# Optimization experiments

Measured on AMD Instinct MI355X. Metric: run time of the kernel, lower is better.

The kernel has to match this reference:

```python
import jax, jax.numpy as jnp
import numpy as np

B, L, H, DK, DV = 4, 2048, 8, 64, 64


def setup_inputs() -> dict:
    key = jax.random.key(0)
    ks = jax.random.split(key, 5)
    s = 0.05
    return {
        "x": jax.random.normal(ks[0], (B, L, DV), dtype=jnp.float32),
        "wq": jax.random.normal(ks[1], (DV, H * DK), dtype=jnp.float32) * s,
        "bq": jnp.zeros((H * DK,), dtype=jnp.float32),
        "wk": jax.random.normal(ks[2], (DV, H * DK), dtype=jnp.float32) * s,
        "bk": jnp.zeros((H * DK,), dtype=jnp.float32),
        "wv": jax.random.normal(ks[3], (DV, H * DV), dtype=jnp.float32) * s,
        "bv": jnp.zeros((H * DV,), dtype=jnp.float32),
        "wo": jax.random.normal(ks[4], (H * DV, DV), dtype=jnp.float32) * s,
        "bo": jnp.zeros((DV,), dtype=jnp.float32),
    }


def reference(x, wq, bq, wk, bk, wv, bv, wo, bo):
    b, l, _ = x.shape
    # QKV projections -> [B, H, L, d]
    q = (x @ wq + bq).reshape(b, l, H, DK).transpose(0, 2, 1, 3)
    k = (x @ wk + bk).reshape(b, l, H, DK).transpose(0, 2, 1, 3)
    v = (x @ wv + bv).reshape(b, l, H, DV).transpose(0, 2, 1, 3)
    # NOTE: original MULTIPLIES by sqrt(dk) (a quirk), not divides.
    align = jnp.einsum('bhqd,bhkd->bhqk', q, k) * jnp.sqrt(jnp.float32(DK))
    align = jax.nn.softmax(align, axis=-1)
    # Equivalent to the tile/multiply/reduce_sum: sum_k align[...,k] * v[...,k,:]
    ctx = jnp.einsum('bhqk,bhkv->bhqv', align, v)  # [B, H, L, DV]
    # NOTE: original transposes to [B, L, DV, H] before flattening (dv-major).
    ctx = ctx.transpose(0, 2, 3, 1).reshape(b, l, DV * H)
    return ctx @ wo + bo
```

## Files before the change

kernel.cpp:

```cpp
#include <hip/hip_runtime.h>


typedef _Float16 half4v __attribute__((ext_vector_type(4)));
typedef _Float16 half8v __attribute__((ext_vector_type(8)));
typedef float    float4v __attribute__((ext_vector_type(4)));

#define BB   4
#define LL   2048
#define HH   8
#define DKV  64
#define NROW (BB * LL)
#define QSCALE 11.541560327111707f

#define KVBLK 64
#define NKB   (LL / KVBLK)

#define GLOAD_LDS(gp, sp) \
    __builtin_amdgcn_global_load_lds((const __attribute__((address_space(1))) void*)(gp), \
                                     (__attribute__((address_space(3))) void*)(sp), 16, 0, 0)

__global__ __launch_bounds__(256) void k_prep_x(const float* __restrict__ x,
                                                _Float16* __restrict__ xh) {
    int i = blockIdx.x * 256 + threadIdx.x;
    float4v v = ((const float4v*)x)[i];
    half4v h;
    h[0] = (_Float16)v[0]; h[1] = (_Float16)v[1];
    h[2] = (_Float16)v[2]; h[3] = (_Float16)v[3];
    ((half4v*)xh)[i] = h;
}

__global__ __launch_bounds__(256) void k_prep_w(const float* __restrict__ wq, const float* __restrict__ bq,
                                                const float* __restrict__ wk, const float* __restrict__ bk,
                                                const float* __restrict__ wv, const float* __restrict__ bv,
                                                _Float16* __restrict__ wt, float* __restrict__ biasc) {
    int idx = blockIdx.x * 256 + threadIdx.x;
    int j = idx >> 6, i = idx & 63;
    const float* w; const float* bsrc; int jj; float sc = 1.0f;
    if (j < 512)       { w = wq; bsrc = bq; jj = j;        sc = QSCALE; }
    else if (j < 1024) { w = wk; bsrc = bk; jj = j - 512;  }
    else               { w = wv; bsrc = bv; jj = j - 1024; }
    wt[idx] = (_Float16)(w[i * 512 + jj] * sc);
    if (i == 0) biasc[j] = bsrc[jj] * sc;
}

__global__ __launch_bounds__(256) void k_prep_wo(const float* __restrict__ wo,
                                                 _Float16* __restrict__ wo2t) {
    int idx = blockIdx.x * 256 + threadIdx.x;
    int j = idx >> 9, k = idx & 511;
    int dv = k & 63, h = k >> 6;
    wo2t[idx] = (_Float16)wo[(dv * HH + h) * 64 + j];
}

__global__ __launch_bounds__(256) void k_proj(const _Float16* __restrict__ xh,
                                              const _Float16* __restrict__ wt,
                                              const float* __restrict__ biasc,
                                              _Float16* __restrict__ qh,
                                              _Float16* __restrict__ kh,
                                              _Float16* __restrict__ vtw) {
    int wid = threadIdx.x >> 6, lane = threadIdx.x & 63;
    int g = lane >> 4, c = lane & 15;
    int m0 = blockIdx.x * 64 + wid * 16;
    int n0 = blockIdx.y * 64;

    half8v a0 = *(const half8v*)(xh + (m0 + c) * 64 + g * 8);
    half8v a1 = *(const half8v*)(xh + (m0 + c) * 64 + 32 + g * 8);

    float4v acc[4] = {};
#pragma unroll
    for (int t = 0; t < 4; ++t) {
        const _Float16* wp = wt + (n0 + t * 16 + c) * 64 + g * 8;
        half8v b0 = *(const half8v*)(wp);
        half8v b1 = *(const half8v*)(wp + 32);
        acc[t] = __builtin_amdgcn_mfma_f32_16x16x32_f16(a0, b0, acc[t], 0, 0, 0);
        acc[t] = __builtin_amdgcn_mfma_f32_16x16x32_f16(a1, b1, acc[t], 0, 0, 0);
    }
#pragma unroll
    for (int t = 0; t < 4; ++t) {
        int j = n0 + t * 16 + c;
        float bias = biasc[j];
        int mat = j >> 9, jj = j & 511, h = jj >> 6;
        if (mat == 2) {
            int b = m0 >> 11, l0 = m0 & 2047;
            half4v hv;
#pragma unroll
            for (int r = 0; r < 4; ++r) hv[r] = (_Float16)(acc[t][r] + bias);
            *(half4v*)(vtw + ((size_t)(b * 8 + h) * 64 + t * 16 + c) * 2048 + l0 + g * 4) = hv;
        } else {
            int cc = (t * 16 + c);
            _Float16* dst = (mat == 0) ? qh : kh;
#pragma unroll
            for (int r = 0; r < 4; ++r) {
                int m = m0 + g * 4 + r;
                int b = m >> 11, l = m & 2047;
                dst[((size_t)(b * HH + h) * LL + l) * 64 + cc] = (_Float16)(acc[t][r] + bias);
            }
        }
    }
}

__global__ __launch_bounds__(512) void k_attn(const _Float16* __restrict__ qh,
                                              const _Float16* __restrict__ kh,
                                              const _Float16* __restrict__ vt,
                                              _Float16* __restrict__ ctx) {
    __shared__ char lds[2 * 16384];

    int tid = threadIdx.x;
    int wid = tid >> 6, lane = tid & 63;
    int g = lane >> 4, c = lane & 15;

    int bid = blockIdx.x;
    int xcd = bid & 7;
    int rest = bid >> 3;
    int bh = xcd * 4 + (rest >> 3);
    int qc = rest & 7;
    int q0 = qc * 256 + wid * 32;

    const _Float16* qp = qh + ((size_t)bh * LL + q0) * 64;
    const char* kg = (const char*)(kh + (size_t)bh * LL * 64);
    const char* vg = (const char*)(vt + (size_t)bh * 64 * LL);

    half8v qa0 = *(const half8v*)(qp + c * 64 + g * 8);
    half8v qa1 = *(const half8v*)(qp + c * 64 + 32 + g * 8);
    half8v qb0 = *(const half8v*)(qp + (16 + c) * 64 + g * 8);
    half8v qb1 = *(const half8v*)(qp + (16 + c) * 64 + 32 + g * 8);

    int pK   = wid * 1024 + lane * 16;
    int rowS = pK >> 7;
    int srcK = (pK & ~127) | ((pK & 127) ^ ((rowS & 7) << 4));
    size_t srcV = (size_t)rowS * (LL * 2) + (size_t)((pK & 127) ^ ((rowS & 7) << 4));

#define STAGE(buf, kb) do {                                                   \
        char* sK = lds + (buf) * 16384 + wid * 1024;                          \
        char* sV = lds + (buf) * 16384 + 8192 + wid * 1024;                   \
        GLOAD_LDS(kg + (size_t)(kb) * 8192 + srcK, sK);                       \
        GLOAD_LDS(vg + srcV + (size_t)(kb) * 128, sV);                        \
    } while (0)

    float4v oa[4] = {}, ob[4] = {};
    float ma = -1e30f, lsumA = 0.0f;
    float mb = -1e30f, lsumB = 0.0f;
    int swzk_c = (c & 7) << 4;

    STAGE(0, 0);

    for (int kb = 0; kb < NKB; ++kb) {
        int cur = kb & 1;
        if (kb + 1 < NKB) {
            STAGE(cur ^ 1, kb + 1);
            asm volatile("s_waitcnt vmcnt(2)" ::: "memory");
        } else {
            asm volatile("s_waitcnt vmcnt(0)" ::: "memory");
        }
        asm volatile("s_barrier" ::: "memory");

        const char* lk = lds + cur * 16384;
        const char* lv = lk + 8192;

#pragma unroll
        for (int s = 0; s < 4; ++s) {
            int krow = s * 16 + c;
            int swzk = (krow & 7) << 4;
            half8v kf0 = *(const half8v*)(lk + krow * 128 + ((g * 16) ^ swzk));
            half8v kf1 = *(const half8v*)(lk + krow * 128 + ((g * 16 + 64) ^ swzk));

            float4v sva = {};
            sva = __builtin_amdgcn_mfma_f32_16x16x32_f16(kf0, qa0, sva, 0, 0, 0);
            sva = __builtin_amdgcn_mfma_f32_16x16x32_f16(kf1, qa1, sva, 0, 0, 0);
            float4v svb = {};
            svb = __builtin_amdgcn_mfma_f32_16x16x32_f16(kf0, qb0, svb, 0, 0, 0);
            svb = __builtin_amdgcn_mfma_f32_16x16x32_f16(kf1, qb1, svb, 0, 0, 0);

            float pmaxa = fmaxf(fmaxf(sva[0], sva[1]), fmaxf(sva[2], sva[3]));
            pmaxa = fmaxf(pmaxa, __shfl_xor(pmaxa, 16));
            pmaxa = fmaxf(pmaxa, __shfl_xor(pmaxa, 32));
            if (__any(pmaxa > ma + 3.0f)) {
                float mn = fmaxf(ma, pmaxa);
                float sc = __builtin_amdgcn_exp2f(ma - mn);
                lsumA *= sc;
#pragma unroll
                for (int t = 0; t < 4; ++t) oa[t] *= sc;
                ma = mn;
            }
            float pa0 = __builtin_amdgcn_exp2f(sva[0] - ma);
            float pa1 = __builtin_amdgcn_exp2f(sva[1] - ma);
            float pa2 = __builtin_amdgcn_exp2f(sva[2] - ma);
            float pa3 = __builtin_amdgcn_exp2f(sva[3] - ma);
            lsumA += (pa0 + pa1) + (pa2 + pa3);
            half4v pha;
            pha[0] = (_Float16)pa0; pha[1] = (_Float16)pa1;
            pha[2] = (_Float16)pa2; pha[3] = (_Float16)pa3;

            float pmaxb = fmaxf(fmaxf(svb[0], svb[1]), fmaxf(svb[2], svb[3]));
            pmaxb = fmaxf(pmaxb, __shfl_xor(pmaxb, 16));
            pmaxb = fmaxf(pmaxb, __shfl_xor(pmaxb, 32));
            if (__any(pmaxb > mb + 3.0f)) {
                float mn = fmaxf(mb, pmaxb);
                float sc = __builtin_amdgcn_exp2f(mb - mn);
                lsumB *= sc;
#pragma unroll
                for (int t = 0; t < 4; ++t) ob[t] *= sc;
                mb = mn;
            }
            float pb0 = __builtin_amdgcn_exp2f(svb[0] - mb);
            float pb1 = __builtin_amdgcn_exp2f(svb[1] - mb);
            float pb2 = __builtin_amdgcn_exp2f(svb[2] - mb);
            float pb3 = __builtin_amdgcn_exp2f(svb[3] - mb);
            lsumB += (pb0 + pb1) + (pb2 + pb3);
            half4v phb;
            phb[0] = (_Float16)pb0; phb[1] = (_Float16)pb1;
            phb[2] = (_Float16)pb2; phb[3] = (_Float16)pb3;

            int vcol = (s * 32 + g * 8) ^ swzk_c;
#pragma unroll
            for (int t = 0; t < 4; ++t) {
                half4v vf = *(const half4v*)(lv + (t * 16 + c) * 128 + vcol);
                oa[t] = __builtin_amdgcn_mfma_f32_16x16x16f16(vf, pha, oa[t], 0, 0, 0);
                ob[t] = __builtin_amdgcn_mfma_f32_16x16x16f16(vf, phb, ob[t], 0, 0, 0);
            }
        }

        asm volatile("s_barrier" ::: "memory");
    }
#undef STAGE

    lsumA += __shfl_xor(lsumA, 16);
    lsumA += __shfl_xor(lsumA, 32);
    lsumB += __shfl_xor(lsumB, 16);
    lsumB += __shfl_xor(lsumB, 32);
    float inva = 1.0f / lsumA;
    float invb = 1.0f / lsumB;

    _Float16* cpa = ctx + ((size_t)bh * LL + q0 + c) * 64 + g * 4;
    _Float16* cpb = cpa + 16 * 64;
#pragma unroll
    for (int t = 0; t < 4; ++t) {
        half4v hva, hvb;
#pragma unroll
        for (int r = 0; r < 4; ++r) {
            hva[r] = (_Float16)(oa[t][r] * inva);
            hvb[r] = (_Float16)(ob[t][r] * invb);
        }
        *(half4v*)(cpa + t * 16) = hva;
        *(half4v*)(cpb + t * 16) = hvb;
    }
}

__global__ __launch_bounds__(64) void k_oproj(const _Float16* __restrict__ ctx,
                                              const _Float16* __restrict__ wo2t,
                                              const float* __restrict__ bo,
                                              float* __restrict__ out) {
    int lane = threadIdx.x & 63;
    int g = lane >> 4, c = lane & 15;
    int m0 = blockIdx.x * 16;
    int b = m0 >> 11, l = m0 & 2047;
    const _Float16* cbase = ctx + ((size_t)b * HH * LL + l) * 64;

    float4v acc[4] = {};
#pragma unroll
    for (int kc = 0; kc < 16; ++kc) {
        int hh = kc >> 1;
        const _Float16* ap = cbase + (size_t)hh * LL * 64 + c * 64 + (kc & 1) * 32 + g * 8;
        half8v a = *(const half8v*)(ap);
#pragma unroll
        for (int t = 0; t < 4; ++t) {
            half8v bf = *(const half8v*)(wo2t + (t * 16 + c) * 512 + kc * 32 + g * 8);
            acc[t] = __builtin_amdgcn_mfma_f32_16x16x32_f16(a, bf, acc[t], 0, 0, 0);
        }
    }
#pragma unroll
    for (int t = 0; t < 4; ++t) {
        float bias = bo[t * 16 + c];
#pragma unroll
        for (int r = 0; r < 4; ++r) {
            int mm = m0 + g * 4 + r;
            out[mm * 64 + t * 16 + c] = acc[t][r] + bias;
        }
    }
}

extern "C" void kernel_launch(void* const* d_in, const int* in_sizes, int n_in,
                              void* d_out, int out_size, void* d_ws, size_t ws_size,
                              hipStream_t stream) {
    const float* x  = (const float*)d_in[0];
    const float* wq = (const float*)d_in[1];
    const float* bq = (const float*)d_in[2];
    const float* wk = (const float*)d_in[3];
    const float* bk = (const float*)d_in[4];
    const float* wv = (const float*)d_in[5];
    const float* bv = (const float*)d_in[6];
    const float* wo = (const float*)d_in[7];
    const float* bo = (const float*)d_in[8];
    float* out = (float*)d_out;

    char* ws = (char*)d_ws;
    _Float16* xh    = (_Float16*)(ws);
    _Float16* wt    = (_Float16*)(ws + 1048576);
    float*    biasc = (float*)   (ws + 1245184);
    _Float16* wo2t  = (_Float16*)(ws + 1251328);
    _Float16* qh    = (_Float16*)(ws + 1316864);
    _Float16* kh    = (_Float16*)(ws + 1316864 + 1ull * 8388608);
    _Float16* vt    = (_Float16*)(ws + 1316864 + 2ull * 8388608);
    _Float16* ctx   = (_Float16*)(ws + 1316864 + 3ull * 8388608);

    hipLaunchKernelGGL(k_prep_x,  dim3(512),      dim3(256), 0, stream, x, xh);
    hipLaunchKernelGGL(k_prep_w,  dim3(384),      dim3(256), 0, stream, wq, bq, wk, bk, wv, bv, wt, biasc);
    hipLaunchKernelGGL(k_prep_wo, dim3(128),      dim3(256), 0, stream, wo, wo2t);
    hipLaunchKernelGGL(k_proj,    dim3(128, 24),  dim3(256), 0, stream, xh, wt, biasc, qh, kh, vt);
    hipLaunchKernelGGL(k_attn,    dim3(256),      dim3(512), 0, stream, qh, kh, vt, ctx);
    hipLaunchKernelGGL(k_oproj,   dim3(512),      dim3(64),  0, stream, ctx, wo2t, bo, out);
}
```

Measured before the change: 115.7 us.

## Split attention KV range across two wave halves and merge partial softmax

Each attention block now covers 128 queries instead of 256. Its eight waves form two halves: each handles 32 queries per wave over half of the key/value sequence (16 blocks each), and the partial max, sum and output are merged through LDS at the end. The grid doubles to 512 blocks so more CUs are occupied on the 256-CU-class device. The cost is doubled LDS per block (64 KB), K/V loaded twice as often per query, and an extra merge step with barriers.

```diff
diff --git a/kernel.cpp b/kernel.cpp
--- a/kernel.cpp
+++ b/kernel.cpp
@@ -13,7 +13,7 @@
 #define QSCALE 11.541560327111707f
 
 #define KVBLK 64
-#define NKB   (LL / KVBLK)
+#define NEP   16
 
 #define GLOAD_LDS(gp, sp) \
     __builtin_amdgcn_global_load_lds((const __attribute__((address_space(1))) void*)(gp), \
@@ -98,22 +98,23 @@
     }
 }
 
-__global__ __launch_bounds__(512) void k_attn(const _Float16* __restrict__ qh,
-                                              const _Float16* __restrict__ kh,
-                                              const _Float16* __restrict__ vt,
-                                              _Float16* __restrict__ ctx) {
-    __shared__ char lds[2 * 16384];
+__global__ __launch_bounds__(512, 4) void k_attn(const _Float16* __restrict__ qh,
+                                                 const _Float16* __restrict__ kh,
+                                                 const _Float16* __restrict__ vt,
+                                                 _Float16* __restrict__ ctx) {
+    __shared__ char lds[2 * 32768];
 
     int tid = threadIdx.x;
     int wid = tid >> 6, lane = tid & 63;
     int g = lane >> 4, c = lane & 15;
+    int qw = wid & 3, half = wid >> 2;
 
     int bid = blockIdx.x;
     int xcd = bid & 7;
     int rest = bid >> 3;
-    int bh = xcd * 4 + (rest >> 3);
-    int qc = rest & 7;
-    int q0 = qc * 256 + wid * 32;
+    int bh = xcd * 4 + (rest >> 4);
+    int qc = rest & 15;
+    int q0 = qc * 128 + qw * 32;
 
     const _Float16* qp = qh + ((size_t)bh * LL + q0) * 64;
     const char* kg = (const char*)(kh + (size_t)bh * LL * 64);
@@ -128,12 +129,14 @@
     int rowS = pK >> 7;
     int srcK = (pK & ~127) | ((pK & 127) ^ ((rowS & 7) << 4));
     size_t srcV = (size_t)rowS * (LL * 2) + (size_t)((pK & 127) ^ ((rowS & 7) << 4));
-
-#define STAGE(buf, kb) do {                                                   \
-        char* sK = lds + (buf) * 16384 + wid * 1024;                          \
-        char* sV = lds + (buf) * 16384 + 8192 + wid * 1024;                   \
-        GLOAD_LDS(kg + (size_t)(kb) * 8192 + srcK, sK);                       \
-        GLOAD_LDS(vg + srcV + (size_t)(kb) * 128, sV);                        \
+    int pDst = wid * 1024;
+
+#define STAGE(buf, e) do {                                                    \
+        char* base = lds + (buf) * 32768;                                     \
+        GLOAD_LDS(kg + (size_t)(e) * 8192 + srcK,        base + pDst);        \
+        GLOAD_LDS(vg + srcV + (size_t)(e) * 128,         base + 8192 + pDst); \
+        GLOAD_LDS(kg + (size_t)(16 + (e)) * 8192 + srcK, base + 16384 + pDst);\
+        GLOAD_LDS(vg + srcV + (size_t)(16 + (e)) * 128,  base + 24576 + pDst);\
     } while (0)
 
     float4v oa[4] = {}, ob[4] = {};
@@ -143,17 +146,17 @@
 
     STAGE(0, 0);
 
-    for (int kb = 0; kb < NKB; ++kb) {
-        int cur = kb & 1;
-        if (kb + 1 < NKB) {
-            STAGE(cur ^ 1, kb + 1);
-            asm volatile("s_waitcnt vmcnt(2)" ::: "memory");
+    for (int e = 0; e < NEP; ++e) {
+        int cur = e & 1;
+        if (e + 1 < NEP) {
+            STAGE(cur ^ 1, e + 1);
+            asm volatile("s_waitcnt vmcnt(4)" ::: "memory");
         } else {
             asm volatile("s_waitcnt vmcnt(0)" ::: "memory");
         }
         asm volatile("s_barrier" ::: "memory");
 
-        const char* lk = lds + cur * 16384;
+        const char* lk = lds + cur * 32768 + half * 16384;
         const char* lv = lk + 8192;
 
 #pragma unroll
@@ -223,25 +226,61 @@
     }
 #undef STAGE
 
-    lsumA += __shfl_xor(lsumA, 16);
-    lsumA += __shfl_xor(lsumA, 32);
-    lsumB += __shfl_xor(lsumB, 16);
-    lsumB += __shfl_xor(lsumB, 32);
-    float inva = 1.0f / lsumA;
-    float invb = 1.0f / lsumB;
-
-    _Float16* cpa = ctx + ((size_t)bh * LL + q0 + c) * 64 + g * 4;
-    _Float16* cpb = cpa + 16 * 64;
-#pragma unroll
-    for (int t = 0; t < 4; ++t) {
-        half4v hva, hvb;
-#pragma unroll
-        for (int r = 0; r < 4; ++r) {
-            hva[r] = (_Float16)(oa[t][r] * inva);
-            hvb[r] = (_Float16)(ob[t][r] * invb);
-        }
-        *(half4v*)(cpa + t * 16) = hva;
-        *(half4v*)(cpb + t * 16) = hvb;
+    __syncthreads();
+    if (half == 1) {
+        float* mr = (float*)(lds + qw * 9216 + lane * 144);
+#pragma unroll
+        for (int t = 0; t < 4; ++t) *(float4v*)(mr + 4 * t) = oa[t];
+#pragma unroll
+        for (int t = 0; t < 4; ++t) *(float4v*)(mr + 16 + 4 * t) = ob[t];
+        float4v sc; sc[0] = ma; sc[1] = lsumA; sc[2] = mb; sc[3] = lsumB;
+        *(float4v*)(mr + 32) = sc;
+    }
+    __syncthreads();
+    if (half == 0) {
+        const float* mr = (const float*)(lds + qw * 9216 + lane * 144);
+        float4v sc = *(const float4v*)(mr + 32);
+        float ma2 = sc[0], la2 = sc[1], mb2 = sc[2], lb2 = sc[3];
+
+        float mMA = fmaxf(ma, ma2);
+        float s1a = __builtin_amdgcn_exp2f(ma - mMA);
+        float s2a = __builtin_amdgcn_exp2f(ma2 - mMA);
+        float mMB = fmaxf(mb, mb2);
+        float s1b = __builtin_amdgcn_exp2f(mb - mMB);
+        float s2b = __builtin_amdgcn_exp2f(mb2 - mMB);
+#pragma unroll
+        for (int t = 0; t < 4; ++t) {
+            float4v o2 = *(const float4v*)(mr + 4 * t);
+            oa[t] = oa[t] * s1a + o2 * s2a;
+        }
+#pragma unroll
+        for (int t = 0; t < 4; ++t) {
+            float4v o2 = *(const float4v*)(mr + 16 + 4 * t);
+            ob[t] = ob[t] * s1b + o2 * s2b;
+        }
+        lsumA = lsumA * s1a + la2 * s2a;
+        lsumB = lsumB * s1b + lb2 * s2b;
+
+        lsumA += __shfl_xor(lsumA, 16);
+        lsumA += __shfl_xor(lsumA, 32);
+        lsumB += __shfl_xor(lsumB, 16);
+        lsumB += __shfl_xor(lsumB, 32);
+        float inva = 1.0f / lsumA;
+        float invb = 1.0f / lsumB;
+
+        _Float16* cpa = ctx + ((size_t)bh * LL + q0 + c) * 64 + g * 4;
+        _Float16* cpb = cpa + 16 * 64;
+#pragma unroll
+        for (int t = 0; t < 4; ++t) {
+            half4v hva, hvb;
+#pragma unroll
+            for (int r = 0; r < 4; ++r) {
+                hva[r] = (_Float16)(oa[t][r] * inva);
+                hvb[r] = (_Float16)(ob[t][r] * invb);
+            }
+            *(half4v*)(cpa + t * 16) = hva;
+            *(half4v*)(cpb + t * 16) = hvb;
+        }
     }
 }
 
@@ -306,6 +345,6 @@
     hipLaunchKernelGGL(k_prep_w,  dim3(384),      dim3(256), 0, stream, wq, bq, wk, bk, wv, bv, wt, biasc);
     hipLaunchKernelGGL(k_prep_wo, dim3(128),      dim3(256), 0, stream, wo, wo2t);
     hipLaunchKernelGGL(k_proj,    dim3(128, 24),  dim3(256), 0, stream, xh, wt, biasc, qh, kh, vt);
-    hipLaunchKernelGGL(k_attn,    dim3(256),      dim3(512), 0, stream, qh, kh, vt, ctx);
+    hipLaunchKernelGGL(k_attn,    dim3(512),      dim3(512), 0, stream, qh, kh, vt, ctx);
     hipLaunchKernelGGL(k_oproj,   dim3(512),      dim3(64),  0, stream, ctx, wo2t, bo, out);
 }
```

Measured after the change: 105.8 us. -8.6%, faster.

## Split KV sequence across waves in attention and merge partial softmax states

Applied to the files above, without the earlier changes.

The attention kernel now launches 1024 blocks of 64 queries instead of 256 blocks of 256 queries. Inside each block, four wave groups each process a different quarter of the KV range in 32-key tiles (split-K). The partial outputs, row maxima and row sums are then merged through LDS in fp16 with log-sum-exp rescaling. The aim is more parallelism and better CU occupancy. In exchange, the per-stage double buffering is replaced by single-buffered synchronous staging with two barriers per step, and the partial outputs are rounded to fp16 before the merge.

```diff
diff --git a/kernel.cpp b/kernel.cpp
--- a/kernel.cpp
+++ b/kernel.cpp
@@ -12,8 +12,8 @@
 #define NROW (BB * LL)
 #define QSCALE 11.541560327111707f
 
-#define KVBLK 64
-#define NKB   (LL / KVBLK)
+#define KVB  32
+#define NEP  16
 
 #define GLOAD_LDS(gp, sp) \
     __builtin_amdgcn_global_load_lds((const __attribute__((address_space(1))) void*)(gp), \
@@ -98,22 +98,23 @@
     }
 }
 
-__global__ __launch_bounds__(512) void k_attn(const _Float16* __restrict__ qh,
-                                              const _Float16* __restrict__ kh,
-                                              const _Float16* __restrict__ vt,
-                                              _Float16* __restrict__ ctx) {
-    __shared__ char lds[2 * 16384];
+__global__ __launch_bounds__(512, 8) void k_attn(const _Float16* __restrict__ qh,
+                                                 const _Float16* __restrict__ kh,
+                                                 const _Float16* __restrict__ vt,
+                                                 _Float16* __restrict__ ctx) {
+    __shared__ char lds[32768];
 
     int tid = threadIdx.x;
     int wid = tid >> 6, lane = tid & 63;
     int g = lane >> 4, c = lane & 15;
+    int qw = wid & 1, half = wid >> 1;
 
     int bid = blockIdx.x;
     int xcd = bid & 7;
     int rest = bid >> 3;
-    int bh = xcd * 4 + (rest >> 3);
-    int qc = rest & 7;
-    int q0 = qc * 256 + wid * 32;
+    int bh = xcd * 4 + (rest >> 5);
+    int qc = rest & 31;
+    int q0 = qc * 64 + qw * 32;
 
     const _Float16* qp = qh + ((size_t)bh * LL + q0) * 64;
     const char* kg = (const char*)(kh + (size_t)bh * LL * 64);
@@ -124,40 +125,40 @@
     half8v qb0 = *(const half8v*)(qp + (16 + c) * 64 + g * 8);
     half8v qb1 = *(const half8v*)(qp + (16 + c) * 64 + 32 + g * 8);
 
-    int pK   = wid * 1024 + lane * 16;
-    int rowS = pK >> 7;
-    int srcK = (pK & ~127) | ((pK & 127) ^ ((rowS & 7) << 4));
-    size_t srcV = (size_t)rowS * (LL * 2) + (size_t)((pK & 127) ^ ((rowS & 7) << 4));
-
-#define STAGE(buf, kb) do {                                                   \
-        char* sK = lds + (buf) * 16384 + wid * 1024;                          \
-        char* sV = lds + (buf) * 16384 + 8192 + wid * 1024;                   \
-        GLOAD_LDS(kg + (size_t)(kb) * 8192 + srcK, sK);                       \
-        GLOAD_LDS(vg + srcV + (size_t)(kb) * 128, sV);                        \
+    int kvw = wid >> 2;
+    int sub = wid & 3;
+    int pS = sub * 1024 + lane * 16;
+    int rK = pS >> 7,  cK = pS & 127;
+    int rV = pS >> 6,  cV = pS & 63;
+    int baseK = rK * 128 + (cK ^ ((rK & 7) << 4));
+    int baseV = rV * 4096 + (cV ^ ((rV & 3) << 4));
+
+#define STAGE(e) do {                                                         \
+        if (kvw == 0) {                                                       \
+            const char* s0 = kg + baseK + (size_t)(e) * 4096;                 \
+            _Pragma("unroll") for (int j = 0; j < 4; ++j)                     \
+                GLOAD_LDS(s0 + j * 65536, lds + (wid + 8 * j) * 1024);        \
+        } else {                                                              \
+            const char* s0 = vg + baseV + (size_t)(e) * 64;                   \
+            _Pragma("unroll") for (int j = 0; j < 4; ++j)                     \
+                GLOAD_LDS(s0 + j * 1024, lds + (wid + 8 * j) * 1024);         \
+        }                                                                     \
     } while (0)
 
     float4v oa[4] = {}, ob[4] = {};
     float ma = -1e30f, lsumA = 0.0f;
     float mb = -1e30f, lsumB = 0.0f;
-    int swzk_c = (c & 7) << 4;
-
-    STAGE(0, 0);
-
-    for (int kb = 0; kb < NKB; ++kb) {
-        int cur = kb & 1;
-        if (kb + 1 < NKB) {
-            STAGE(cur ^ 1, kb + 1);
-            asm volatile("s_waitcnt vmcnt(2)" ::: "memory");
-        } else {
-            asm volatile("s_waitcnt vmcnt(0)" ::: "memory");
-        }
-        asm volatile("s_barrier" ::: "memory");
-
-        const char* lk = lds + cur * 16384;
-        const char* lv = lk + 8192;
-
-#pragma unroll
-        for (int s = 0; s < 4; ++s) {
+
+    STAGE(0);
+
+    const char* lk = lds + half * 8192;
+    const char* lv = lk + 4096;
+
+    for (int e = 0; e < NEP; ++e) {
+        __syncthreads();
+
+#pragma unroll
+        for (int s = 0; s < 2; ++s) {
             int krow = s * 16 + c;
             int swzk = (krow & 7) << 4;
             half8v kf0 = *(const half8v*)(lk + krow * 128 + ((g * 16) ^ swzk));
@@ -170,7 +171,7 @@
             svb = __builtin_amdgcn_mfma_f32_16x16x32_f16(kf0, qb0, svb, 0, 0, 0);
             svb = __builtin_amdgcn_mfma_f32_16x16x32_f16(kf1, qb1, svb, 0, 0, 0);
 
-            float pmaxa = fmaxf(fmaxf(sva[0], sva[1]), fmaxf(sva[2], sva[3]));
+            float pmaxa = fmaxf(fmaxf(fmaxf(sva[0], sva[1]), sva[2]), sva[3]);
             pmaxa = fmaxf(pmaxa, __shfl_xor(pmaxa, 16));
             pmaxa = fmaxf(pmaxa, __shfl_xor(pmaxa, 32));
             if (__any(pmaxa > ma + 3.0f)) {
@@ -190,7 +191,7 @@
             pha[0] = (_Float16)pa0; pha[1] = (_Float16)pa1;
             pha[2] = (_Float16)pa2; pha[3] = (_Float16)pa3;
 
-            float pmaxb = fmaxf(fmaxf(svb[0], svb[1]), fmaxf(svb[2], svb[3]));
+            float pmaxb = fmaxf(fmaxf(fmaxf(svb[0], svb[1]), svb[2]), svb[3]);
             pmaxb = fmaxf(pmaxb, __shfl_xor(pmaxb, 16));
             pmaxb = fmaxf(pmaxb, __shfl_xor(pmaxb, 32));
             if (__any(pmaxb > mb + 3.0f)) {
@@ -210,38 +211,84 @@
             phb[0] = (_Float16)pb0; phb[1] = (_Float16)pb1;
             phb[2] = (_Float16)pb2; phb[3] = (_Float16)pb3;
 
-            int vcol = (s * 32 + g * 8) ^ swzk_c;
+            int vcol = (s * 32 + g * 8) ^ ((c & 3) << 4);
 #pragma unroll
             for (int t = 0; t < 4; ++t) {
-                half4v vf = *(const half4v*)(lv + (t * 16 + c) * 128 + vcol);
+                half4v vf = *(const half4v*)(lv + (t * 16 + c) * 64 + vcol);
                 oa[t] = __builtin_amdgcn_mfma_f32_16x16x16f16(vf, pha, oa[t], 0, 0, 0);
                 ob[t] = __builtin_amdgcn_mfma_f32_16x16x16f16(vf, phb, ob[t], 0, 0, 0);
             }
         }
 
-        asm volatile("s_barrier" ::: "memory");
+        if (e + 1 < NEP) {
+            __syncthreads();
+            STAGE(e + 1);
+        }
     }
 #undef STAGE
 
-    lsumA += __shfl_xor(lsumA, 16);
-    lsumA += __shfl_xor(lsumA, 32);
-    lsumB += __shfl_xor(lsumB, 16);
-    lsumB += __shfl_xor(lsumB, 32);
-    float inva = 1.0f / lsumA;
-    float invb = 1.0f / lsumB;
-
-    _Float16* cpa = ctx + ((size_t)bh * LL + q0 + c) * 64 + g * 4;
-    _Float16* cpb = cpa + 16 * 64;
-#pragma unroll
-    for (int t = 0; t < 4; ++t) {
-        half4v hva, hvb;
-#pragma unroll
-        for (int r = 0; r < 4; ++r) {
-            hva[r] = (_Float16)(oa[t][r] * inva);
-            hvb[r] = (_Float16)(ob[t][r] * invb);
-        }
-        *(half4v*)(cpa + t * 16) = hva;
-        *(half4v*)(cpb + t * 16) = hvb;
+    __syncthreads();
+    if (half != 0) {
+        char* mr = ((char*)lds) + (((half - 1) * 2 + qw) * 64 + lane) * 80;
+#pragma unroll
+        for (int t = 0; t < 4; ++t) {
+            half4v ha, hb;
+#pragma unroll
+            for (int r = 0; r < 4; ++r) { ha[r] = (_Float16)oa[t][r]; hb[r] = (_Float16)ob[t][r]; }
+            *(half4v*)(mr + t * 8) = ha;
+            *(half4v*)(mr + 32 + t * 8) = hb;
+        }
+        float4v sc;
+        sc[0] = ma; sc[1] = lsumA; sc[2] = mb; sc[3] = lsumB;
+        *(float4v*)(mr + 64) = sc;
+    }
+    __syncthreads();
+    if (half == 0) {
+#pragma unroll
+        for (int j = 1; j <= 3; ++j) {
+            const char* mr = ((const char*)lds) + (((j - 1) * 2 + qw) * 64 + lane) * 80;
+            float4v sc = *(const float4v*)(mr + 64);
+            float mNA = fmaxf(ma, sc[0]);
+            float s1a = __builtin_amdgcn_exp2f(ma - mNA);
+            float s2a = __builtin_amdgcn_exp2f(sc[0] - mNA);
+            float mNB = fmaxf(mb, sc[2]);
+            float s1b = __builtin_amdgcn_exp2f(mb - mNB);
+            float s2b = __builtin_amdgcn_exp2f(sc[2] - mNB);
+#pragma unroll
+            for (int t = 0; t < 4; ++t) {
+                half4v ha = *(const half4v*)(mr + t * 8);
+                half4v hb = *(const half4v*)(mr + 32 + t * 8);
+#pragma unroll
+                for (int r = 0; r < 4; ++r) {
+                    oa[t][r] = oa[t][r] * s1a + (float)ha[r] * s2a;
+                    ob[t][r] = ob[t][r] * s1b + (float)hb[r] * s2b;
+                }
+            }
+            lsumA = lsumA * s1a + sc[1] * s2a;
+            lsumB = lsumB * s1b + sc[3] * s2b;
+            ma = mNA; mb = mNB;
+        }
+
+        lsumA += __shfl_xor(lsumA, 16);
+        lsumA += __shfl_xor(lsumA, 32);
+        lsumB += __shfl_xor(lsumB, 16);
+        lsumB += __shfl_xor(lsumB, 32);
+        float inva = 1.0f / lsumA;
+        float invb = 1.0f / lsumB;
+
+        _Float16* cpa = ctx + ((size_t)bh * LL + q0 + c) * 64 + g * 4;
+        _Float16* cpb = cpa + 16 * 64;
+#pragma unroll
+        for (int t = 0; t < 4; ++t) {
+            half4v hva, hvb;
+#pragma unroll
+            for (int r = 0; r < 4; ++r) {
+                hva[r] = (_Float16)(oa[t][r] * inva);
+                hvb[r] = (_Float16)(ob[t][r] * invb);
+            }
+            *(half4v*)(cpa + t * 16) = hva;
+            *(half4v*)(cpb + t * 16) = hvb;
+        }
     }
 }
 
@@ -306,6 +353,6 @@
     hipLaunchKernelGGL(k_prep_w,  dim3(384),      dim3(256), 0, stream, wq, bq, wk, bk, wv, bv, wt, biasc);
     hipLaunchKernelGGL(k_prep_wo, dim3(128),      dim3(256), 0, stream, wo, wo2t);
     hipLaunchKernelGGL(k_proj,    dim3(128, 24),  dim3(256), 0, stream, xh, wt, biasc, qh, kh, vt);
-    hipLaunchKernelGGL(k_attn,    dim3(256),      dim3(512), 0, stream, qh, kh, vt, ctx);
+    hipLaunchKernelGGL(k_attn,    dim3(1024),     dim3(512), 0, stream, qh, kh, vt, ctx);
     hipLaunchKernelGGL(k_oproj,   dim3(512),      dim3(64),  0, stream, ctx, wo2t, bo, out);
 }
```

Measured after the change: 284.6 us. 2.46x slower.
